# Kernel tuning notes

Hardware: AMD Instinct MI355X
Metric: run time of the kernel (lower is better)

Reference implementation:

```python
import jax, jax.numpy as jnp
import numpy as np

IN_F = 512
OUT_F = 512

def setup_inputs() -> dict:
    key = jax.random.key(0)
    k1, k2, k3 = jax.random.split(key, 3)
    x = jax.random.normal(k1, (2, 512, IN_F), dtype=jnp.float32)
    # uniform init: a = sqrt(6 / (2 + out_features))
    a = float(np.sqrt(6.0 / (2.0 + OUT_F)))
    W = jax.random.uniform(k2, (OUT_F, IN_F), dtype=jnp.float32, minval=-a, maxval=a)
    bound = float(1.0 / np.sqrt(IN_F))
    b = jax.random.uniform(k3, (OUT_F,), dtype=jnp.float32, minval=-bound, maxval=bound)
    return {"x": x, "W": W, "b": b}

def reference(x, W, b):
    # MAM fully connected (beta == 0 path): for each (row, out-neuron),
    # C = max_k(x_k * w_ok) + min_k(x_k * w_ok), then add bias.
    xf = x.reshape(-1, x.shape[-1])            # (B, in)
    prod = xf[:, None, :] * W[None, :, :]      # (B, out, in) -- the large intermediate
    C = prod.max(axis=-1) + prod.min(axis=-1)  # (B, out)
    C = C + b[None, :]
    return C.reshape(x.shape[:-1] + (W.shape[0],))
```

## Files before the change

kernel.cpp:

```cpp
#include <hip/hip_runtime.h>
#include <math.h>


#define O_TOTAL 512
#define K_TOTAL 512
#define OBLK 64
#define NWAVE 4
#define RPW 4
#define RPB (NWAVE * RPW)
#define KCH 64
#define NCHUNK (K_TOTAL / KCH)

__global__ __launch_bounds__(256, 2)
void mam_fc_kernel(const float* __restrict__ x, const float* __restrict__ W,
                   const float* __restrict__ bias, float* __restrict__ out) {
  __shared__ float Wl[2][OBLK * KCH];

  const int t = threadIdx.x;
  const int lane = t & 63;
  const int wv = __builtin_amdgcn_readfirstlane(t >> 6);
  const int ob = blockIdx.x & 7;
  const int rg = blockIdx.x >> 3;
  const int o0 = ob * OBLK;
  const int rowBase = rg * RPB + wv * RPW;

  const int s_or = t >> 4;
  const int s_g  = t & 15;

  const float* Wg = W + (size_t)o0 * K_TOTAL;
  const float* xr0 = x + (size_t)rowBase * K_TOTAL;

  float amax[RPW][2], amin[RPW][2];
#pragma unroll
  for (int r = 0; r < RPW; ++r) {
#pragma unroll
    for (int p = 0; p < 2; ++p) { amax[r][p] = -INFINITY; amin[r][p] = INFINITY; }
  }

#pragma unroll
  for (int i = 0; i < 4; ++i) {
    const int o_l = s_or + 16 * i;
    const float4 v = *reinterpret_cast<const float4*>(Wg + (size_t)o_l * K_TOTAL + s_g * 4);
    const int gsw = s_g ^ (o_l & 15);
    *reinterpret_cast<float4*>(&Wl[0][o_l * KCH + gsw * 4]) = v;
  }
  __syncthreads();

#pragma unroll 1
  for (int c = 0; c < NCHUNK; ++c) {
    if (c + 1 < NCHUNK) {
      const int kc2 = (c + 1) * KCH;
      float* dst = Wl[(c + 1) & 1];
#pragma unroll
      for (int i = 0; i < 4; ++i) {
        const int o_l = s_or + 16 * i;
        const float4 v = *reinterpret_cast<const float4*>(Wg + (size_t)o_l * K_TOTAL + kc2 + s_g * 4);
        const int gsw = s_g ^ (o_l & 15);
        *reinterpret_cast<float4*>(&dst[o_l * KCH + gsw * 4]) = v;
      }
    }

    const float* buf = Wl[c & 1];
    const int kc = c * KCH;
#pragma unroll
    for (int j = 0; j < KCH / 4; ++j) {
      const float4 w4 = *reinterpret_cast<const float4*>(
          &buf[lane * KCH + ((j ^ (lane & 15)) * 4)]);
      const int par = j & 1;
#pragma unroll
      for (int r = 0; r < RPW; ++r) {
        const float4 x4 = *reinterpret_cast<const float4*>(
            xr0 + (size_t)r * K_TOTAL + kc + j * 4);
        const float p0 = x4.x * w4.x;
        const float p1 = x4.y * w4.y;
        const float p2 = x4.z * w4.z;
        const float p3 = x4.w * w4.w;
        amax[r][par] = fmaxf(fmaxf(fmaxf(fmaxf(amax[r][par], p0), p1), p2), p3);
        amin[r][par] = fminf(fminf(fminf(fminf(amin[r][par], p0), p1), p2), p3);
      }
    }
    __syncthreads();
  }

  const float bv = bias[o0 + lane];
#pragma unroll
  for (int r = 0; r < RPW; ++r) {
    const float m = fmaxf(amax[r][0], amax[r][1]);
    const float n = fminf(amin[r][0], amin[r][1]);
    out[(size_t)(rowBase + r) * O_TOTAL + (o0 + lane)] = m + n + bv;
  }
}

extern "C" void kernel_launch(void* const* d_in, const int* in_sizes, int n_in,
                              void* d_out, int out_size, void* d_ws, size_t ws_size,
                              hipStream_t stream) {
  const float* x = (const float*)d_in[0];
  const float* W = (const float*)d_in[1];
  const float* b = (const float*)d_in[2];
  float* out = (float*)d_out;

  const int nrows = in_sizes[0] / K_TOTAL;
  const int nblocks = (O_TOTAL / OBLK) * (nrows / RPB);
  mam_fc_kernel<<<dim3(nblocks), dim3(256), 0, stream>>>(x, W, b, out);
}
```

Baseline: 24.29 us.

## Stage W and x via direct global-to-LDS loads, halve rows per wave

Replaces the register round-trip W staging with global_load_lds direct-to-LDS copies, and also stages x rows into a double-buffered LDS tile instead of reading them per-lane from global memory. Rows per wave drop from 4 to 2, which doubles the grid, and the occupancy hint rises to 4 blocks per CU. This is meant to cut VGPR pressure and global load latency in the inner loop and to raise parallelism, at the cost of less W reuse per block and more LDS per block. The only wait before each LDS read is __syncthreads, so correctness depends on that barrier also draining the async direct-to-LDS loads.

```diff
diff --git a/kernel.cpp b/kernel.cpp
--- a/kernel.cpp
+++ b/kernel.cpp
@@ -6,15 +6,27 @@
 #define K_TOTAL 512
 #define OBLK 64
 #define NWAVE 4
-#define RPW 4
+#define RPW 2
 #define RPB (NWAVE * RPW)
 #define KCH 64
 #define NCHUNK (K_TOTAL / KCH)
 
-__global__ __launch_bounds__(256, 2)
+__device__ __forceinline__ void stage16(const float* g, float* lds, int lane) {
+#if __has_builtin(__builtin_amdgcn_global_load_lds)
+  (void)lane;
+  __builtin_amdgcn_global_load_lds(
+      (__attribute__((address_space(1))) unsigned int*)g,
+      (__attribute__((address_space(3))) unsigned int*)lds, 16, 0, 0);
+#else
+  *reinterpret_cast<float4*>(lds + lane * 4) = *reinterpret_cast<const float4*>(g);
+#endif
+}
+
+__global__ __launch_bounds__(256, 4)
 void mam_fc_kernel(const float* __restrict__ x, const float* __restrict__ W,
                    const float* __restrict__ bias, float* __restrict__ out) {
   __shared__ float Wl[2][OBLK * KCH];
+  __shared__ float Xl[2][RPB * KCH];
 
   const int t = threadIdx.x;
   const int lane = t & 63;
@@ -22,13 +34,19 @@
   const int ob = blockIdx.x & 7;
   const int rg = blockIdx.x >> 3;
   const int o0 = ob * OBLK;
-  const int rowBase = rg * RPB + wv * RPW;
+  const int rowBase = rg * RPB;
 
-  const int s_or = t >> 4;
-  const int s_g  = t & 15;
-
-  const float* Wg = W + (size_t)o0 * K_TOTAL;
-  const float* xr0 = x + (size_t)rowBase * K_TOTAL;
+  const float* srcW[4];
+  int dstWoff[4];
+#pragma unroll
+  for (int p = 0; p < 4; ++p) {
+    const int orow = wv * 16 + p * 4 + (lane >> 4);
+    const int g = (lane & 15) ^ (orow & 15);
+    srcW[p] = W + (size_t)(o0 + orow) * K_TOTAL + g * 4;
+    dstWoff[p] = (wv * 16 + p * 4) * KCH;
+  }
+  const float* srcX = x + (size_t)(rowBase + wv * 4 + (lane >> 4)) * K_TOTAL + (lane & 15) * 4;
+  const int dstXoff = wv * 4 * KCH;
 
   float amax[RPW][2], amin[RPW][2];
 #pragma unroll
@@ -37,44 +55,37 @@
     for (int p = 0; p < 2; ++p) { amax[r][p] = -INFINITY; amin[r][p] = INFINITY; }
   }
 
+  const unsigned baseW = (unsigned)(lane * (KCH * 4) + (lane & 15) * 16);
+  const unsigned baseX = (unsigned)((wv * RPW) * (KCH * 4));
+
 #pragma unroll
-  for (int i = 0; i < 4; ++i) {
-    const int o_l = s_or + 16 * i;
-    const float4 v = *reinterpret_cast<const float4*>(Wg + (size_t)o_l * K_TOTAL + s_g * 4);
-    const int gsw = s_g ^ (o_l & 15);
-    *reinterpret_cast<float4*>(&Wl[0][o_l * KCH + gsw * 4]) = v;
-  }
+  for (int p = 0; p < 4; ++p) stage16(srcW[p], &Wl[0][dstWoff[p]], lane);
+  if (wv < 2) stage16(srcX, &Xl[0][dstXoff], lane);
   __syncthreads();
 
 #pragma unroll 1
   for (int c = 0; c < NCHUNK; ++c) {
     if (c + 1 < NCHUNK) {
-      const int kc2 = (c + 1) * KCH;
-      float* dst = Wl[(c + 1) & 1];
+      const int b = (c + 1) & 1;
+      const int kOff = (c + 1) * KCH;
 #pragma unroll
-      for (int i = 0; i < 4; ++i) {
-        const int o_l = s_or + 16 * i;
-        const float4 v = *reinterpret_cast<const float4*>(Wg + (size_t)o_l * K_TOTAL + kc2 + s_g * 4);
-        const int gsw = s_g ^ (o_l & 15);
-        *reinterpret_cast<float4*>(&dst[o_l * KCH + gsw * 4]) = v;
-      }
+      for (int p = 0; p < 4; ++p) stage16(srcW[p] + kOff, &Wl[b][dstWoff[p]], lane);
+      if (wv < 2) stage16(srcX + kOff, &Xl[b][dstXoff], lane);
     }
 
-    const float* buf = Wl[c & 1];
-    const int kc = c * KCH;
+    const char* wb = (const char*)&Wl[c & 1][0];
+    const char* xb = (const char*)&Xl[c & 1][0];
 #pragma unroll
     for (int j = 0; j < KCH / 4; ++j) {
-      const float4 w4 = *reinterpret_cast<const float4*>(
-          &buf[lane * KCH + ((j ^ (lane & 15)) * 4)]);
-      const int par = j & 1;
+      const float4 w4 = *reinterpret_cast<const float4*>(wb + (baseW ^ (unsigned)(j * 16)));
 #pragma unroll
       for (int r = 0; r < RPW; ++r) {
-        const float4 x4 = *reinterpret_cast<const float4*>(
-            xr0 + (size_t)r * K_TOTAL + kc + j * 4);
+        const float4 x4 = *reinterpret_cast<const float4*>(xb + baseX + r * (KCH * 4) + j * 16);
         const float p0 = x4.x * w4.x;
         const float p1 = x4.y * w4.y;
         const float p2 = x4.z * w4.z;
         const float p3 = x4.w * w4.w;
+        const int par = j & 1;
         amax[r][par] = fmaxf(fmaxf(fmaxf(fmaxf(amax[r][par], p0), p1), p2), p3);
         amin[r][par] = fminf(fminf(fminf(fminf(amin[r][par], p0), p1), p2), p3);
       }
@@ -85,9 +96,9 @@
   const float bv = bias[o0 + lane];
 #pragma unroll
   for (int r = 0; r < RPW; ++r) {
-    const float m = fmaxf(amax[r][0], amax[r][1]);
-    const float n = fminf(amin[r][0], amin[r][1]);
-    out[(size_t)(rowBase + r) * O_TOTAL + (o0 + lane)] = m + n + bv;
+    const float mm = fmaxf(amax[r][0], amax[r][1]);
+    const float nn = fminf(amin[r][0], amin[r][1]);
+    out[(size_t)(rowBase + wv * RPW + r) * O_TOTAL + o0 + lane] = mm + nn + bv;
   }
 }
 
```

Result: faster. 22.08 us (-9.1%).
